# Performance work log

Hardware: AMD Instinct MI355X
Metric: run time of the kernel (lower is better)

The kernel has to match this reference:

```python
import jax, jax.numpy as jnp
import numpy as np

B = 4096
OBS_DIM = 1024
E_OUT = 512
H1 = 2048
H2 = 2048


def setup_inputs() -> dict:
    key = jax.random.key(0)
    ks = jax.random.split(key, 12)
    def kaiming(k, shape, fan_in):
        return jax.random.normal(k, shape, dtype=jnp.float32) * np.float32(np.sqrt(2.0 / fan_in))
    obs = jax.random.normal(ks[0], (B, OBS_DIM), dtype=jnp.float32)
    # lineare: Linear(obs_dim, e_outputs), torch weight shape [out, in]
    We = kaiming(ks[1], (E_OUT, OBS_DIM), OBS_DIM)
    be = jax.random.normal(ks[2], (E_OUT,), dtype=jnp.float32) * 0.01
    # obs_dim attention heads, each Linear(e_outputs, 2), stacked
    attn_W = kaiming(ks[3], (OBS_DIM, E_OUT, 2), E_OUT)
    attn_b = jax.random.normal(ks[4], (OBS_DIM, 2), dtype=jnp.float32) * 0.01
    # v_net: Linear(obs_dim,H1)+tanh, Linear(H1,H2)+[dropout(eval:no-op)]+tanh, Linear(H2,1)
    W1 = kaiming(ks[5], (H1, OBS_DIM), OBS_DIM)
    b1 = jnp.zeros((H1,), dtype=jnp.float32)
    W2 = kaiming(ks[6], (H2, H1), H1)
    b2 = jnp.zeros((H2,), dtype=jnp.float32)
    W3 = kaiming(ks[7], (1, H2), H2)
    b3 = jnp.zeros((1,), dtype=jnp.float32)
    return {"obs": obs, "We": We, "be": be, "attn_W": attn_W, "attn_b": attn_b,
            "W1": W1, "b1": b1, "W2": W2, "b2": b2, "W3": W3, "b3": b3}


def reference(obs, We, be, attn_W, attn_b, W1, b1, W2, b2, W3, b3):
    # e = tanh(lineare(obs)) : [B, E_OUT]
    e = jnp.tanh(obs @ We.T + be)
    # all obs_dim attention heads batched into one contraction: [B, OBS_DIM, 2]
    logits = jnp.einsum('be,oec->boc', e, attn_W) + attn_b
    # softmax over the 2 logits, keep prob of class 1 -> Attention [B, OBS_DIM]
    attention = jax.nn.softmax(logits, axis=-1)[..., 1]
    state_attention = obs * attention
    # v_net (eval mode: dropout is identity)
    h = jnp.tanh(state_attention @ W1.T + b1)
    h = jnp.tanh(h @ W2.T + b2)
    v = jnp.squeeze(h @ W3.T + b3, -1)  # [B]
    return (v, attention)
```

## Files before the change

### kernel.cpp

```cpp
#include <hip/hip_runtime.h>
#include <hip/hip_bf16.h>

typedef unsigned short u16;
typedef u16 u16x4 __attribute__((ext_vector_type(4)));
typedef u16 u16x8 __attribute__((ext_vector_type(8)));
typedef __bf16 bf16x8 __attribute__((ext_vector_type(8)));
typedef float f32x4 __attribute__((ext_vector_type(4)));

__device__ __forceinline__ u16 f2bf(float f) {
  unsigned u = __float_as_uint(f);
  u += 0x7FFFu + ((u >> 16) & 1u);
  return (u16)(u >> 16);
}
__device__ __forceinline__ float bf2f(u16 h) {
  return __uint_as_float(((unsigned)h) << 16);
}
__device__ __forceinline__ float tanh_fast(float x) {
  float t = __expf(2.0f * x);
  return 1.0f - 2.0f / (t + 1.0f);
}
__device__ __forceinline__ float sigmoid_fast(float x) {
  return 1.0f / (1.0f + __expf(-x));
}

__device__ __forceinline__ void cvt4(const float* __restrict__ s, u16* __restrict__ d, int q) {
  float4 v = ((const float4*)s)[q];
  u16x4 o = { f2bf(v.x), f2bf(v.y), f2bf(v.z), f2bf(v.w) };
  ((u16x4*)d)[q] = o;
}

__global__ __launch_bounds__(256)
void prep_kernel(const float* __restrict__ obs, const float* __restrict__ We,
                 const float* __restrict__ W1, const float* __restrict__ W2,
                 const float* __restrict__ aW, const float* __restrict__ ab,
                 u16* __restrict__ obs_b, u16* __restrict__ We_b,
                 u16* __restrict__ W1_b, u16* __restrict__ W2_b,
                 u16* __restrict__ Wd, float* __restrict__ bd,
                 float* __restrict__ vzero) {
  int q = blockIdx.x * 256 + threadIdx.x;
  if (q < 1024) ((float4*)vzero)[q] = (float4){0.f, 0.f, 0.f, 0.f};
  if (q < 1048576) { cvt4(obs, obs_b, q); return; }
  q -= 1048576;
  if (q < 131072) { cvt4(We, We_b, q); return; }
  q -= 131072;
  if (q < 524288) { cvt4(W1, W1_b, q); return; }
  q -= 524288;
  if (q < 1048576) { cvt4(W2, W2_b, q); return; }
  q -= 1048576;
  if (q < 131072) {
    int i0 = q * 4;
    int o = i0 >> 9, e0 = i0 & 511;
    const float* p = aW + (size_t)o * 1024 + e0 * 2;
    float4 v0 = *(const float4*)p;
    float4 v1 = *(const float4*)(p + 4);
    u16x4 od = { f2bf(v0.y - v0.x), f2bf(v0.w - v0.z),
                 f2bf(v1.y - v1.x), f2bf(v1.w - v1.z) };
    *(u16x4*)(Wd + i0) = od;
    if (q < 256) {
      float4 a0 = *(const float4*)(ab + q * 8);
      float4 a1 = *(const float4*)(ab + q * 8 + 4);
      float4 ob = { a0.y - a0.x, a0.w - a0.z, a1.y - a1.x, a1.w - a1.z };
      *(float4*)(bd + q * 4) = ob;
    }
  }
}

template <int BM, int BN, int EP>
__global__ __launch_bounds__(256, 2)
void gemm_bt(const u16* __restrict__ A, const u16* __restrict__ Bt,
             int N, int K,
             const float* __restrict__ bias,
             u16* __restrict__ outb, float* __restrict__ outf,
             const u16* __restrict__ obsb, u16* __restrict__ sa,
             const float* __restrict__ W3, const float* __restrict__ b3,
             float* __restrict__ vout) {
  constexpr int LS = 72;
  constexpr int CA = BM / 32;
  constexpr int CB = BN / 32;
  constexpr int MI = BM / 32;
  constexpr int NJ = BN / 32;

  __shared__ __align__(16) u16 As[BM * LS];
  __shared__ __align__(16) u16 Bs[BN * LS];

  const int tid = threadIdx.x;
  const int lane = tid & 63;
  const int wave = tid >> 6;
  const int bm = blockIdx.x, bn = blockIdx.y;

  const int r0 = tid >> 3;
  const int kc = (tid & 7) * 8;

  const u16* gA[CA];
  const u16* gB[CB];
#pragma unroll
  for (int q = 0; q < CA; ++q)
    gA[q] = A + (size_t)(bm * BM + r0 + q * 32) * K + kc;
#pragma unroll
  for (int q = 0; q < CB; ++q)
    gB[q] = Bt + (size_t)(bn * BN + r0 + q * 32) * K + kc;

  u16x8 pa[CA], pb[CB];
#pragma unroll
  for (int q = 0; q < CA; ++q) { pa[q] = *(const u16x8*)gA[q]; gA[q] += 64; }
#pragma unroll
  for (int q = 0; q < CB; ++q) { pb[q] = *(const u16x8*)gB[q]; gB[q] += 64; }

  const int wm = (wave >> 1) * (BM / 2);
  const int wn = (wave & 1) * (BN / 2);
  const int fr = lane & 15;
  const int koff = (lane >> 4) * 8;

  f32x4 acc[MI][NJ];
#pragma unroll
  for (int i = 0; i < MI; ++i)
#pragma unroll
    for (int j = 0; j < NJ; ++j)
      acc[i][j] = (f32x4){0.f, 0.f, 0.f, 0.f};

  const int T = K >> 6;
  for (int k = 0; k < T; ++k) {
    __syncthreads();
#pragma unroll
    for (int q = 0; q < CA; ++q) *(u16x8*)(As + (r0 + q * 32) * LS + kc) = pa[q];
#pragma unroll
    for (int q = 0; q < CB; ++q) *(u16x8*)(Bs + (r0 + q * 32) * LS + kc) = pb[q];
    __syncthreads();

    if (k + 1 < T) {
#pragma unroll
      for (int q = 0; q < CA; ++q) { pa[q] = *(const u16x8*)gA[q]; gA[q] += 64; }
#pragma unroll
      for (int q = 0; q < CB; ++q) { pb[q] = *(const u16x8*)gB[q]; gB[q] += 64; }
    }

#pragma unroll
    for (int s = 0; s < 2; ++s) {
      bf16x8 a[MI], b[NJ];
#pragma unroll
      for (int i = 0; i < MI; ++i)
        a[i] = *(const bf16x8*)(As + (wm + i * 16 + fr) * LS + s * 32 + koff);
#pragma unroll
      for (int j = 0; j < NJ; ++j)
        b[j] = *(const bf16x8*)(Bs + (wn + j * 16 + fr) * LS + s * 32 + koff);
#pragma unroll
      for (int i = 0; i < MI; ++i)
#pragma unroll
        for (int j = 0; j < NJ; ++j)
          acc[i][j] = __builtin_amdgcn_mfma_f32_16x16x32_bf16(a[i], b[j], acc[i][j], 0, 0, 0);
    }
  }

  if constexpr (EP == 2) {
    float vpart[MI][4];
#pragma unroll
    for (int i = 0; i < MI; ++i)
#pragma unroll
      for (int r = 0; r < 4; ++r) vpart[i][r] = 0.f;
#pragma unroll
    for (int j = 0; j < NJ; ++j) {
      const int col = bn * BN + wn + j * 16 + fr;
      const float bv = bias[col];
      const float w3 = W3[col];
#pragma unroll
      for (int i = 0; i < MI; ++i)
#pragma unroll
        for (int r = 0; r < 4; ++r)
          vpart[i][r] += tanh_fast(acc[i][j][r] + bv) * w3;
    }
    const bool lead = (fr == 0);
    const bool addb = (bn == 0) && ((wave & 1) == 0);
#pragma unroll
    for (int i = 0; i < MI; ++i)
#pragma unroll
      for (int r = 0; r < 4; ++r) {
        float p = vpart[i][r];
        p += __shfl_xor(p, 8);
        p += __shfl_xor(p, 4);
        p += __shfl_xor(p, 2);
        p += __shfl_xor(p, 1);
        if (lead) {
          const int row = bm * BM + wm + i * 16 + (lane >> 4) * 4 + r;
          atomicAdd(vout + row, addb ? p + b3[0] : p);
        }
      }
  } else {
#pragma unroll
    for (int j = 0; j < NJ; ++j) {
      const int col = bn * BN + wn + j * 16 + fr;
      const float bv = bias[col];
#pragma unroll
      for (int i = 0; i < MI; ++i) {
#pragma unroll
        for (int r = 0; r < 4; ++r) {
          const int row = bm * BM + wm + i * 16 + (lane >> 4) * 4 + r;
          const float x = acc[i][j][r] + bv;
          const size_t idx = (size_t)row * N + col;
          if constexpr (EP == 0) {
            outb[idx] = f2bf(tanh_fast(x));
          } else {
            const float att = sigmoid_fast(x);
            outf[idx] = att;
            sa[idx] = f2bf(bf2f(obsb[idx]) * att);
          }
        }
      }
    }
  }
}

extern "C" void kernel_launch(void* const* d_in, const int* in_sizes, int n_in,
                              void* d_out, int out_size, void* d_ws, size_t ws_size,
                              hipStream_t stream) {
  const float* obs   = (const float*)d_in[0];
  const float* We    = (const float*)d_in[1];
  const float* be    = (const float*)d_in[2];
  const float* attnW = (const float*)d_in[3];
  const float* attnb = (const float*)d_in[4];
  const float* W1    = (const float*)d_in[5];
  const float* b1    = (const float*)d_in[6];
  const float* W2    = (const float*)d_in[7];
  const float* b2    = (const float*)d_in[8];
  const float* W3    = (const float*)d_in[9];
  const float* b3    = (const float*)d_in[10];
  float* out = (float*)d_out;

  char* ws = (char*)d_ws;
  u16*   We_b  = (u16*)(ws + 0x00000000);
  u16*   Wd_b  = (u16*)(ws + 0x00100000);
  u16*   W1_b  = (u16*)(ws + 0x00200000);
  u16*   W2_b  = (u16*)(ws + 0x00600000);
  float* bd    = (float*)(ws + 0x00E00000);
  u16*   obs_b = (u16*)(ws + 0x00E01000);
  u16*   e_b   = (u16*)(ws + 0x01601000);
  u16*   sa_b  = (u16*)(ws + 0x01A01000);
  u16*   h1_b  = (u16*)(ws + 0x02201000);

  prep_kernel<<<11264, 256, 0, stream>>>(obs, We, W1, W2, attnW, attnb,
                                         obs_b, We_b, W1_b, W2_b, Wd_b, bd, out);

  gemm_bt<64, 64, 0><<<dim3(64, 8), 256, 0, stream>>>(
      obs_b, We_b, 512, 1024, be, e_b, nullptr, nullptr, nullptr, nullptr, nullptr, nullptr);
  gemm_bt<128, 64, 1><<<dim3(32, 16), 256, 0, stream>>>(
      e_b, Wd_b, 1024, 512, bd, nullptr, out + 4096, obs_b, sa_b, nullptr, nullptr, nullptr);
  gemm_bt<128, 128, 0><<<dim3(32, 16), 256, 0, stream>>>(
      sa_b, W1_b, 2048, 1024, b1, h1_b, nullptr, nullptr, nullptr, nullptr, nullptr, nullptr);
  gemm_bt<128, 128, 2><<<dim3(32, 16), 256, 0, stream>>>(
      h1_b, W2_b, 2048, 2048, b2, nullptr, nullptr, nullptr, nullptr, W3, b3, out);
}
```

Before: 204.5 us.

## Load GEMM tiles directly into LDS with global_load_lds and raise occupancy

The GEMM kernel no longer stages A/B tiles through registers. It now issues 16-byte global_load_lds transfers straight into unpadded 64-wide LDS tiles, and the launch-bounds occupancy hint rises from 2 to 4 blocks. This saves VGPRs and the ds_write instructions, letting more blocks hide latency. In exchange, the register-level prefetch of the next tile is gone, so global latency is no longer overlapped within a block. Dropping the row padding may also cause LDS bank conflicts on the fragment reads.

```diff
diff --git a/kernel.cpp b/kernel.cpp
--- a/kernel.cpp
+++ b/kernel.cpp
@@ -21,6 +21,12 @@
 }
 __device__ __forceinline__ float sigmoid_fast(float x) {
   return 1.0f / (1.0f + __expf(-x));
+}
+
+__device__ __forceinline__ void glds16(const u16* g, u16* l) {
+  __builtin_amdgcn_global_load_lds(
+      (const __attribute__((address_space(1))) unsigned int*)g,
+      (__attribute__((address_space(3))) unsigned int*)l, 16, 0, 0);
 }
 
 __device__ __forceinline__ void cvt4(const float* __restrict__ s, u16* __restrict__ d, int q) {
@@ -66,7 +72,7 @@
 }
 
 template <int BM, int BN, int EP>
-__global__ __launch_bounds__(256, 2)
+__global__ __launch_bounds__(256, 4)
 void gemm_bt(const u16* __restrict__ A, const u16* __restrict__ Bt,
              int N, int K,
              const float* __restrict__ bias,
@@ -74,14 +80,13 @@
              const u16* __restrict__ obsb, u16* __restrict__ sa,
              const float* __restrict__ W3, const float* __restrict__ b3,
              float* __restrict__ vout) {
-  constexpr int LS = 72;
   constexpr int CA = BM / 32;
   constexpr int CB = BN / 32;
   constexpr int MI = BM / 32;
   constexpr int NJ = BN / 32;
 
-  __shared__ __align__(16) u16 As[BM * LS];
-  __shared__ __align__(16) u16 Bs[BN * LS];
+  __shared__ __align__(16) u16 As[BM * 64];
+  __shared__ __align__(16) u16 Bs[BN * 64];
 
   const int tid = threadIdx.x;
   const int lane = tid & 63;
@@ -91,20 +96,10 @@
   const int r0 = tid >> 3;
   const int kc = (tid & 7) * 8;
 
-  const u16* gA[CA];
-  const u16* gB[CB];
-#pragma unroll
-  for (int q = 0; q < CA; ++q)
-    gA[q] = A + (size_t)(bm * BM + r0 + q * 32) * K + kc;
-#pragma unroll
-  for (int q = 0; q < CB; ++q)
-    gB[q] = Bt + (size_t)(bn * BN + r0 + q * 32) * K + kc;
-
-  u16x8 pa[CA], pb[CB];
-#pragma unroll
-  for (int q = 0; q < CA; ++q) { pa[q] = *(const u16x8*)gA[q]; gA[q] += 64; }
-#pragma unroll
-  for (int q = 0; q < CB; ++q) { pb[q] = *(const u16x8*)gB[q]; gB[q] += 64; }
+  const u16* gA = A + (size_t)(bm * BM + r0) * K + kc;
+  const u16* gB = Bt + (size_t)(bn * BN + r0) * K + kc;
+  u16* lA = As + r0 * 64 + kc;
+  u16* lB = Bs + r0 * 64 + kc;
 
   const int wm = (wave >> 1) * (BM / 2);
   const int wn = (wave & 1) * (BN / 2);
@@ -120,29 +115,25 @@
 
   const int T = K >> 6;
   for (int k = 0; k < T; ++k) {
+    if (k) __syncthreads();
+#pragma unroll
+    for (int q = 0; q < CA; ++q)
+      glds16(gA + (size_t)q * 32 * K, lA + q * 32 * 64);
+#pragma unroll
+    for (int q = 0; q < CB; ++q)
+      glds16(gB + (size_t)q * 32 * K, lB + q * 32 * 64);
+    gA += 64; gB += 64;
     __syncthreads();
-#pragma unroll
-    for (int q = 0; q < CA; ++q) *(u16x8*)(As + (r0 + q * 32) * LS + kc) = pa[q];
-#pragma unroll
-    for (int q = 0; q < CB; ++q) *(u16x8*)(Bs + (r0 + q * 32) * LS + kc) = pb[q];
-    __syncthreads();
-
-    if (k + 1 < T) {
-#pragma unroll
-      for (int q = 0; q < CA; ++q) { pa[q] = *(const u16x8*)gA[q]; gA[q] += 64; }
-#pragma unroll
-      for (int q = 0; q < CB; ++q) { pb[q] = *(const u16x8*)gB[q]; gB[q] += 64; }
-    }
 
 #pragma unroll
     for (int s = 0; s < 2; ++s) {
       bf16x8 a[MI], b[NJ];
 #pragma unroll
       for (int i = 0; i < MI; ++i)
-        a[i] = *(const bf16x8*)(As + (wm + i * 16 + fr) * LS + s * 32 + koff);
+        a[i] = *(const bf16x8*)(As + (wm + i * 16 + fr) * 64 + s * 32 + koff);
 #pragma unroll
       for (int j = 0; j < NJ; ++j)
-        b[j] = *(const bf16x8*)(Bs + (wn + j * 16 + fr) * LS + s * 32 + koff);
+        b[j] = *(const bf16x8*)(Bs + (wn + j * 16 + fr) * 64 + s * 32 + koff);
 #pragma unroll
       for (int i = 0; i < MI; ++i)
 #pragma unroll
```

Measured after the change: 222.9 us. +9.0%, slower.
